# Performance work log

Measured on AMD Instinct MI355X. Metric: run time of the kernel, lower is better.

## Reference

```python
import jax, jax.numpy as jnp
import numpy as np

N, D, K = 32768, 256, 4096
COMMITMENT_COST = 0.25
EPS_NORM = 1e-12  # matches torch F.normalize eps


def _l2_normalize(x):
    n = jnp.linalg.norm(x, axis=1, keepdims=True)
    return x / jnp.maximum(n, EPS_NORM)


def setup_inputs() -> dict:
    key = jax.random.key(0)
    k1, k2 = jax.random.split(key)
    inputs = jax.random.normal(k1, (N, D), dtype=jnp.float32)
    # xavier_uniform-like scale for the codebook
    bound = float(np.sqrt(6.0 / (K + D)))
    embeddings = jax.random.uniform(k2, (K, D), dtype=jnp.float32, minval=-bound, maxval=bound)
    return {"inputs": inputs, "embeddings": embeddings}


def reference(inputs, embeddings):
    flat = inputs.reshape(-1, D)
    x = _l2_normalize(flat)              # [N, D]
    e = _l2_normalize(embeddings)        # [K, D]
    # squared euclidean distance on normalized vectors
    distances = (jnp.sum(x * x, axis=1, keepdims=True)
                 + jnp.sum(e * e, axis=1)
                 - 2.0 * jnp.matmul(x, e.T))          # [N, K]
    encoding_indices = jnp.argmin(distances, axis=1)  # [N]
    quantized = embeddings[encoding_indices]          # gather, [N, D]
    # commitment loss (EMA variant: only commitment term is trained)
    e_latent_loss = jnp.mean((jax.lax.stop_gradient(quantized) - flat) ** 2)
    loss = COMMITMENT_COST * e_latent_loss
    # straight-through estimator
    quantized_st = flat + jax.lax.stop_gradient(quantized - flat)
    quantized_st = quantized_st.reshape(inputs.shape)
    return quantized_st, loss, encoding_indices
```

## Files before the change

### kernel.cpp

```cpp
#include <hip/hip_runtime.h>
#include <math.h>
#include <stdint.h>
#include <limits.h>

#define NPTS 32768
#define DIM  256
#define KCB  4096
#define NQ   (NPTS*DIM)

#define EPSN    1e-12f
#define MARGIN1 6.0e-4f
#define F16MIN  6.103515625e-05f
#define CAPB    4096
#define KINIT   0x7F800000FFFFFFFFull

typedef __attribute__((ext_vector_type(8))) _Float16 f16x8;
typedef __attribute__((ext_vector_type(4))) _Float16 f16x4;
typedef __attribute__((ext_vector_type(4))) float    f32x4;

#define WS_EH0   0u
#define WS_TRI   2097152u
#define WS_SUME  4194304u
#define WS_EINV  4210688u
#define WS_XINV  4227072u
#define WS_IDX   4358144u
#define WS_RCB   4489216u
#define WS_RLB   4489232u
#define WS_BEST  4505616u
#define WS_LOSSP 4915232u

__device__ inline unsigned fbits(float f){ union{float f;unsigned u;}v; v.f=f; return v.u; }
__device__ inline float bitsf(unsigned u){ union{float f;unsigned u;}v; v.u=u; return v.f; }
__device__ inline uint64_t dbits(double d){ union{double d;uint64_t u;}v; v.d=d; return v.u; }
__device__ inline _Float16 g16(float v){
    return (fabsf(v) < F16MIN) ? (_Float16)0.0f : (_Float16)v;
}
__device__ inline void gload16(const void* src, void* lds){
    __builtin_amdgcn_global_load_lds((const __attribute__((address_space(1))) void*)src,
                                     (__attribute__((address_space(3))) void*)lds, 16, 0, 0);
}

__global__ __launch_bounds__(256) void k_norm(const float* __restrict__ x,
                                              const float* __restrict__ e,
                                              float* __restrict__ xinv,
                                              _Float16* __restrict__ eh0,
                                              float* __restrict__ sume,
                                              float* __restrict__ einv,
                                              int* __restrict__ rcb,
                                              uint64_t* __restrict__ bestu) {
    int w = threadIdx.x >> 6, l = threadIdx.x & 63;
    if (blockIdx.x < NPTS/4) {
        int row = blockIdx.x * 4 + w;
        float4 v = ((const float4*)x)[row * 64 + l];
        float s = v.x*v.x + v.y*v.y + v.z*v.z + v.w*v.w;
        #pragma unroll
        for (int o = 32; o; o >>= 1) s += __shfl_xor(s, o);
        if (l == 0) xinv[row] = 1.0f / fmaxf(sqrtf(s), EPSN);
    } else {
        int eb = blockIdx.x - NPTS/4;
        if (eb == 0 && threadIdx.x == 0) *rcb = 0;
        if (eb < 16) bestu[eb * 256 + threadIdx.x] = ~0ull;
        int row = eb * 4 + w;
        float4 v = ((const float4*)e)[row * 64 + l];
        float s = v.x*v.x + v.y*v.y + v.z*v.z + v.w*v.w;
        #pragma unroll
        for (int o = 32; o; o >>= 1) s += __shfl_xor(s, o);
        float inv = 1.0f / fmaxf(sqrtf(s), EPSN);
        float4 n = make_float4(v.x*inv, v.y*inv, v.z*inv, v.w*inv);
        f16x4 h0; h0[0]=g16(n.x); h0[1]=g16(n.y); h0[2]=g16(n.z); h0[3]=g16(n.w);
        ((f16x4*)eh0)[row * 64 + l] = h0;
        float s2 = n.x*n.x + n.y*n.y + n.z*n.z + n.w*n.w;
        #pragma unroll
        for (int o = 32; o; o >>= 1) s2 += __shfl_xor(s2, o);
        if (l == 0) { sume[row] = s2; einv[row] = inv; }
    }
}

__global__ __launch_bounds__(256,2) void k_phase1(
    const float* __restrict__ x, const float* __restrict__ xinv,
    const _Float16* __restrict__ eh0,
    ulonglong2* __restrict__ tri)
{
    __shared__ __align__(16) _Float16 Bs[2][32 * DIM];
    const int tid = threadIdx.x;
    const int w = tid >> 6, l = tid & 63;
    const int l15 = l & 15, lhi = l >> 4;
    const int rowbase = (blockIdx.x >> 2) * 256 + w * 64;
    const int kbase   = (blockIdx.x & 3) * 1024;
    char* BsC = (char*)&Bs[0][0];

    f16x8 a[4][8];
    #pragma unroll
    for (int g = 0; g < 4; g++) {
        int row = rowbase + g*16 + l15;
        float xv = xinv[row];
        const float4* xr = (const float4*)(x + row * DIM);
        #pragma unroll
        for (int dc = 0; dc < 8; dc++) {
            float4 f0 = xr[dc*8 + lhi*2];
            float4 f1 = xr[dc*8 + lhi*2 + 1];
            f16x8 av;
            av[0]=g16(f0.x*xv); av[1]=g16(f0.y*xv);
            av[2]=g16(f0.z*xv); av[3]=g16(f0.w*xv);
            av[4]=g16(f1.x*xv); av[5]=g16(f1.y*xv);
            av[6]=g16(f1.z*xv); av[7]=g16(f1.w*xv);
            a[g][dc] = av;
        }
    }

    uint64_t t0[4], t1[4];
    float d2[4];
    #pragma unroll
    for (int g = 0; g < 4; g++) { t0[g]=KINIT; t1[g]=KINIT; d2[g]=INFINITY; }

    const char* sbase = (const char*)eh0 + (size_t)kbase * 512
                      + (size_t)(l & 31) * 512 + w*32 + (l >> 5)*16;
    auto stage = [&](int kt, int bufbyte) {
        const char* s = sbase + kt * 16384;
        #pragma unroll
        for (int p = 0; p < 4; p++) {
            gload16(s + p*128, BsC + bufbyte + ((p*256 + w*64) << 4));
        }
    };

    const int rb = lhi*512 + l15*16;
    const f32x4 zc = (f32x4){0.f, 0.f, 0.f, 0.f};

    auto compute = [&](int kt, int bufbyte) {
        f32x4 acc[4][2];
        #pragma unroll
        for (int dc = 0; dc < 8; dc++) {
            #pragma unroll
            for (int ni = 0; ni < 2; ni++) {
                f16x8 b = *(const f16x8*)(BsC + bufbyte + dc*2048 + ni*256 + rb);
                if (dc == 0) {
                    acc[0][ni] = __builtin_amdgcn_mfma_f32_16x16x32_f16(b, a[0][0], zc, 0, 0, 0);
                    acc[1][ni] = __builtin_amdgcn_mfma_f32_16x16x32_f16(b, a[1][0], zc, 0, 0, 0);
                    acc[2][ni] = __builtin_amdgcn_mfma_f32_16x16x32_f16(b, a[2][0], zc, 0, 0, 0);
                    acc[3][ni] = __builtin_amdgcn_mfma_f32_16x16x32_f16(b, a[3][0], zc, 0, 0, 0);
                } else {
                    acc[0][ni] = __builtin_amdgcn_mfma_f32_16x16x32_f16(b, a[0][dc], acc[0][ni], 0, 0, 0);
                    acc[1][ni] = __builtin_amdgcn_mfma_f32_16x16x32_f16(b, a[1][dc], acc[1][ni], 0, 0, 0);
                    acc[2][ni] = __builtin_amdgcn_mfma_f32_16x16x32_f16(b, a[2][dc], acc[2][ni], 0, 0, 0);
                    acc[3][ni] = __builtin_amdgcn_mfma_f32_16x16x32_f16(b, a[3][dc], acc[3][ni], 0, 0, 0);
                }
            }
        }

        #pragma unroll
        for (int ni = 0; ni < 2; ni++) {
            #pragma unroll
            for (int g = 0; g < 4; g++) {
                f32x4 v = acc[g][ni];
                float mx = fmaxf(fmaxf(v[0], v[1]), fmaxf(v[2], v[3]));
                if (5.0f - 2.0f*mx < d2[g]) {
                    #pragma unroll
                    for (int r = 0; r < 4; r++) {
                        float db = 5.0f - 2.0f*v[r];
                        if (db < d2[g]) {
                            int code = kbase + kt*32 + ni*16 + lhi*4 + r;
                            uint64_t key = ((uint64_t)fbits(db) << 32) | (unsigned)code;
                            if (key < t1[g]) {
                                d2[g] = bitsf((unsigned)(t1[g] >> 32));
                                if (key < t0[g]) { t1[g] = t0[g]; t0[g] = key; }
                                else t1[g] = key;
                            } else {
                                d2[g] = db;
                            }
                        }
                    }
                }
            }
        }
    };

    stage(0, 0);
    for (int kt = 0; kt < 32; kt += 2) {
        __syncthreads();
        stage(kt + 1, 16384);
        compute(kt, 0);
        __syncthreads();
        if (kt + 2 < 32) stage(kt + 2, 0);
        compute(kt + 1, 16384);
    }

    #pragma unroll
    for (int g = 0; g < 4; g++) {
        uint64_t a0 = t0[g], a1 = t1[g];
        float a2 = d2[g];
        #pragma unroll
        for (int m = 16; m < 64; m <<= 1) {
            uint64_t b0 = __shfl_xor(a0, m), b1 = __shfl_xor(a1, m);
            float    b2 = __shfl_xor(a2, m);
            uint64_t lo  = a0 < b0 ? a0 : b0;
            uint64_t hi0 = a0 < b0 ? b0 : a0;
            uint64_t lo1 = a1 < b1 ? a1 : b1;
            uint64_t mid = hi0 > lo1 ? hi0 : lo1;
            a1 = hi0 < lo1 ? hi0 : lo1;
            a0 = lo;
            a2 = fminf(fminf(a2, b2), bitsf((unsigned)(mid >> 32)));
        }
        t0[g] = a0; t1[g] = a1; d2[g] = a2;
    }

    if (lhi == 0) {
        const int split = blockIdx.x & 3;
        #pragma unroll
        for (int g = 0; g < 4; g++) {
            int row = rowbase + g*16 + l15;
            float d0 = bitsf((unsigned)(t0[g] >> 32));
            uint64_t flag = (d2[g] - d0 < MARGIN1) ? (1ull << 12) : 0ull;
            ulonglong2 ent;
            ent.x = t0[g];
            ent.y = t1[g] | flag;
            tri[(row << 2) | split] = ent;
        }
    }
}

__global__ __launch_bounds__(256) void k_tailA(
    const ulonglong2* __restrict__ tri,
    const float* __restrict__ x, const float* __restrict__ emb,
    const float* __restrict__ xinv, const float* __restrict__ einv,
    const float* __restrict__ sume,
    int* __restrict__ idx,
    int* __restrict__ rcb, int* __restrict__ rlb)
{
    __shared__ int rowsA[256], ksA[256];
    __shared__ int cntA;
    const int tid = threadIdx.x;
    if (tid == 0) cntA = 0;
    __syncthreads();

    {
        int row = blockIdx.x * 256 + tid;
        ulonglong2 e0 = tri[row*4+0], e1 = tri[row*4+1],
                   e2 = tri[row*4+2], e3 = tri[row*4+3];
        uint64_t c0 = e0.x, c1 = e0.y & ~0x1000ull;
        float c2 = INFINITY;
        auto fold = [&](uint64_t b0, uint64_t b1) {
            b1 &= ~0x1000ull;
            uint64_t lo  = c0 < b0 ? c0 : b0;
            uint64_t hi0 = c0 < b0 ? b0 : c0;
            uint64_t lo1 = c1 < b1 ? c1 : b1;
            uint64_t mid = hi0 > lo1 ? hi0 : lo1;
            c1 = hi0 < lo1 ? hi0 : lo1;
            c0 = lo;
            c2 = fminf(c2, bitsf((unsigned)(mid >> 32)));
        };
        fold(e1.x, e1.y); fold(e2.x, e2.y); fold(e3.x, e3.y);
        int k0 = (int)((unsigned)c0 & 0xFFFu);
        idx[row] = k0;
        float d0 = bitsf((unsigned)(c0 >> 32));
        float d1 = bitsf((unsigned)(c1 >> 32));
        bool lA = (d1 - d0 < MARGIN1);
        bool lB = (c2 - d0 < MARGIN1);
        if ((e0.y >> 12) & 1) lB |= (bitsf((unsigned)(e0.x >> 32)) - d0 < MARGIN1);
        if ((e1.y >> 12) & 1) lB |= (bitsf((unsigned)(e1.x >> 32)) - d0 < MARGIN1);
        if ((e2.y >> 12) & 1) lB |= (bitsf((unsigned)(e2.x >> 32)) - d0 < MARGIN1);
        if ((e3.y >> 12) & 1) lB |= (bitsf((unsigned)(e3.x >> 32)) - d0 < MARGIN1);
        if (lA) {
            int k1 = (int)((unsigned)c1 & 0xFFFu);
            int p = atomicAdd(&cntA, 1);
            rowsA[p] = row; ksA[p] = k0 | (k1 << 12);
        }
        if (lB) {
            int q = atomicAdd(rcb, 1);
            if (q < CAPB) rlb[q] = row;
        }
    }
    __syncthreads();

    const int w = tid >> 6, l = tid & 63;
    const int nA = cntA;
    for (int i = w; i < nA; i += 4) {
        int row = rowsA[i];
        int k0 = ksA[i] & 0xFFF, k1 = (ksA[i] >> 12) & 0xFFF;
        float xv = xinv[row];
        float4 xf = ((const float4*)x)[row * 64 + l];
        double x0 = (double)xf.x * (double)xv, x1 = (double)xf.y * (double)xv;
        double x2 = (double)xf.z * (double)xv, x3 = (double)xf.w * (double)xv;
        int ks[2] = {k0, k1};
        double d[2];
        #pragma unroll
        for (int c = 0; c < 2; c++) {
            int k = ks[c];
            float ev = einv[k];
            float4 e4 = ((const float4*)emb)[k * 64 + l];
            d[c] = x0 * (double)(e4.x * ev) + x1 * (double)(e4.y * ev)
                 + x2 * (double)(e4.z * ev) + x3 * (double)(e4.w * ev);
        }
        #pragma unroll
        for (int o = 32; o; o >>= 1) {
            d[0] += __shfl_xor(d[0], o);
            d[1] += __shfl_xor(d[1], o);
        }
        if (l == 0) {
            double dist0 = 4.0 + (double)sume[k0] - 2.0 * d[0];
            double dist1 = 4.0 + (double)sume[k1] - 2.0 * d[1];
            uint64_t key0 = (dbits(dist0) & 0xFFFFFFFFFFFFF000ull) | (unsigned)k0;
            uint64_t key1 = (dbits(dist1) & 0xFFFFFFFFFFFFF000ull) | (unsigned)k1;
            idx[row] = (int)((key0 < key1 ? key0 : key1) & 0xFFFull);
        }
    }
}

__global__ __launch_bounds__(256) void k_full(
    const float* __restrict__ x, const float* __restrict__ emb,
    const float* __restrict__ xinv, const float* __restrict__ einv,
    const float* __restrict__ sume,
    const int* __restrict__ rcb, const int* __restrict__ rlb,
    uint64_t* __restrict__ bestu)
{
    __shared__ __align__(16) float xs[DIM];
    int cnt = *rcb; if (cnt > CAPB) cnt = CAPB; if (cnt <= 0) return;
    const int tid = threadIdx.x;
    const int grp = tid >> 3, sub = tid & 7;
    int items = cnt * 16;
    for (int item = blockIdx.x; item < items; item += gridDim.x) {
        int r = item >> 4, chunk = item & 15;
        int row = rlb[r];
        __syncthreads();
        xs[tid] = x[row * DIM + tid] * xinv[row];
        __syncthreads();
        const float4* xs4 = (const float4*)xs;
        uint64_t best = ~0ull;
        #pragma unroll
        for (int j = 0; j < 8; j++) {
            int k = chunk * 256 + grp * 8 + j;
            float ev = einv[k];
            const float4* e4 = (const float4*)(emb + (size_t)k * DIM);
            double dp0 = 0, dp1 = 0;
            #pragma unroll
            for (int i = 0; i < 8; i += 2) {
                float4 ef0 = e4[sub + i*8];
                float4 xf0 = xs4[sub + i*8];
                float4 ef1 = e4[sub + (i+1)*8];
                float4 xf1 = xs4[sub + (i+1)*8];
                dp0 += (double)xf0.x * (double)(ef0.x * ev)
                     + (double)xf0.y * (double)(ef0.y * ev)
                     + (double)xf0.z * (double)(ef0.z * ev)
                     + (double)xf0.w * (double)(ef0.w * ev);
                dp1 += (double)xf1.x * (double)(ef1.x * ev)
                     + (double)xf1.y * (double)(ef1.y * ev)
                     + (double)xf1.z * (double)(ef1.z * ev)
                     + (double)xf1.w * (double)(ef1.w * ev);
            }
            double dp = dp0 + dp1;
            #pragma unroll
            for (int o = 4; o; o >>= 1) dp += __shfl_xor(dp, o);
            if (sub == 0) {
                double dist = 4.0 + (double)sume[k] - 2.0 * dp;
                uint64_t key = (dbits(dist) & 0xFFFFFFFFFFFFF000ull) | (unsigned)k;
                best = key < best ? key : best;
            }
        }
        if (sub == 0)
            atomicMin((unsigned long long*)&bestu[r], (unsigned long long)best);
    }
}

__global__ __launch_bounds__(256) void k_ffin(const int* __restrict__ rcb,
                                              const int* __restrict__ rlb,
                                              const uint64_t* __restrict__ bestu,
                                              int* __restrict__ idx) {
    int cnt = *rcb; if (cnt > CAPB) cnt = CAPB;
    int i = blockIdx.x * 256 + threadIdx.x;
    if (i < cnt) idx[rlb[i]] = (int)(bestu[i] & 0xFFFull);
}

__global__ __launch_bounds__(256) void k_gather(const float* __restrict__ x,
                                                const float* __restrict__ emb,
                                                const int* __restrict__ idx,
                                                float* __restrict__ out,
                                                float* __restrict__ lossp) {
    int t = blockIdx.x * 256 + threadIdx.x;
    float ls = 0.f;
    #pragma unroll
    for (int s = 0; s < 4; ++s) {
        int i4 = t + s * 524288;
        int n = i4 >> 6, c4 = i4 & 63;
        int id = idx[n];
        float4 f = ((const float4*)x)[i4];
        float4 q = ((const float4*)emb)[id * 64 + c4];
        float dx = q.x - f.x, dy = q.y - f.y, dz = q.z - f.z, dw = q.w - f.w;
        float4 o = make_float4(f.x + dx, f.y + dy, f.z + dz, f.w + dw);
        ((float4*)out)[i4] = o;
        ls += dx*dx + dy*dy + dz*dz + dw*dw;
        if (c4 == 0) out[NQ + 1 + n] = (float)id;
    }
    #pragma unroll
    for (int o = 32; o; o >>= 1) ls += __shfl_xor(ls, o);
    __shared__ float wsum[4];
    int wid = threadIdx.x >> 6, lane = threadIdx.x & 63;
    if (lane == 0) wsum[wid] = ls;
    __syncthreads();
    if (threadIdx.x == 0) lossp[blockIdx.x] = wsum[0] + wsum[1] + wsum[2] + wsum[3];
}

__global__ __launch_bounds__(256) void k_finalize(const float* __restrict__ lossp,
                                                  float* __restrict__ out) {
    double s = 0;
    for (int i = threadIdx.x; i < 2048; i += 256) s += (double)lossp[i];
    #pragma unroll
    for (int o = 32; o; o >>= 1) s += __shfl_xor(s, o);
    __shared__ double wd[4];
    int wid = threadIdx.x >> 6, lane = threadIdx.x & 63;
    if (lane == 0) wd[wid] = s;
    __syncthreads();
    if (threadIdx.x == 0)
        out[NQ] = (float)(0.25 * ((wd[0] + wd[1] + wd[2] + wd[3]) / (double)NQ));
}

extern "C" void kernel_launch(void* const* d_in, const int* in_sizes, int n_in,
                              void* d_out, int out_size, void* d_ws, size_t ws_size,
                              hipStream_t stream) {
    const float* x   = (const float*)d_in[0];
    const float* emb = (const float*)d_in[1];
    char* ws = (char*)d_ws;
    _Float16* eh0 = (_Float16*)(ws + WS_EH0);
    ulonglong2* tri = (ulonglong2*)(ws + WS_TRI);
    float* sume  = (float*)(ws + WS_SUME);
    float* einv  = (float*)(ws + WS_EINV);
    float* xinv  = (float*)(ws + WS_XINV);
    int*   idx   = (int*)  (ws + WS_IDX);
    int*   rcb   = (int*)  (ws + WS_RCB);
    int*   rlb   = (int*)  (ws + WS_RLB);
    uint64_t* bestu = (uint64_t*)(ws + WS_BEST);
    float* lossp = (float*)(ws + WS_LOSSP);
    float* out = (float*)d_out;

    hipLaunchKernelGGL(k_norm,     dim3(NPTS/4 + KCB/4), dim3(256), 0, stream,
                       x, emb, xinv, eh0, sume, einv, rcb, bestu);
    hipLaunchKernelGGL(k_phase1,   dim3(NPTS/256*4),     dim3(256), 0, stream,
                       x, xinv, eh0, tri);
    hipLaunchKernelGGL(k_tailA,    dim3(NPTS/256),       dim3(256), 0, stream,
                       tri, x, emb, xinv, einv, sume, idx, rcb, rlb);
    hipLaunchKernelGGL(k_full,     dim3(2048),           dim3(256), 0, stream,
                       x, emb, xinv, einv, sume, rcb, rlb, bestu);
    hipLaunchKernelGGL(k_ffin,     dim3(16),             dim3(256), 0, stream, rcb, rlb, bestu, idx);
    hipLaunchKernelGGL(k_gather,   dim3(2048),           dim3(256), 0, stream,
                       x, emb, idx, out, lossp);
    hipLaunchKernelGGL(k_finalize, dim3(1),              dim3(256), 0, stream, lossp, out);
}
```

Baseline: 171.5 us.

## Precompute fp16 normalized inputs and split codebook search eight ways

Adds an fp16 copy of the normalized input rows, written by the norm kernel into the output buffer as scratch, so phase1 loads fp16 fragments directly instead of reloading fp32 and converting. Phase1 now splits the codebook into eight 512-code slices instead of four, doubling the block count to improve occupancy and load balance. The per-row partial results also move into the output buffer and are merged over eight entries in tailA. This trades extra scratch traffic and a longer merge for more parallelism, and relies on the output buffer being overwritten later by k_gather.

```diff
diff --git a/kernel.cpp b/kernel.cpp
--- a/kernel.cpp
+++ b/kernel.cpp
@@ -13,13 +13,13 @@
 #define F16MIN  6.103515625e-05f
 #define CAPB    4096
 #define KINIT   0x7F800000FFFFFFFFull
+#define NSPLIT  8
 
 typedef __attribute__((ext_vector_type(8))) _Float16 f16x8;
 typedef __attribute__((ext_vector_type(4))) _Float16 f16x4;
 typedef __attribute__((ext_vector_type(4))) float    f32x4;
 
 #define WS_EH0   0u
-#define WS_TRI   2097152u
 #define WS_SUME  4194304u
 #define WS_EINV  4210688u
 #define WS_XINV  4227072u
@@ -28,6 +28,7 @@
 #define WS_RLB   4489232u
 #define WS_BEST  4505616u
 #define WS_LOSSP 4915232u
+#define DOUT_TRI 16777216u
 
 __device__ inline unsigned fbits(float f){ union{float f;unsigned u;}v; v.f=f; return v.u; }
 __device__ inline float bitsf(unsigned u){ union{float f;unsigned u;}v; v.u=u; return v.f; }
@@ -43,6 +44,7 @@
 __global__ __launch_bounds__(256) void k_norm(const float* __restrict__ x,
                                               const float* __restrict__ e,
                                               float* __restrict__ xinv,
+                                              _Float16* __restrict__ xh,
                                               _Float16* __restrict__ eh0,
                                               float* __restrict__ sume,
                                               float* __restrict__ einv,
@@ -55,7 +57,11 @@
         float s = v.x*v.x + v.y*v.y + v.z*v.z + v.w*v.w;
         #pragma unroll
         for (int o = 32; o; o >>= 1) s += __shfl_xor(s, o);
-        if (l == 0) xinv[row] = 1.0f / fmaxf(sqrtf(s), EPSN);
+        float inv = 1.0f / fmaxf(sqrtf(s), EPSN);
+        if (l == 0) xinv[row] = inv;
+        f16x4 h;
+        h[0]=g16(v.x*inv); h[1]=g16(v.y*inv); h[2]=g16(v.z*inv); h[3]=g16(v.w*inv);
+        ((f16x4*)xh)[row * 64 + l] = h;
     } else {
         int eb = blockIdx.x - NPTS/4;
         if (eb == 0 && threadIdx.x == 0) *rcb = 0;
@@ -77,7 +83,7 @@
 }
 
 __global__ __launch_bounds__(256,2) void k_phase1(
-    const float* __restrict__ x, const float* __restrict__ xinv,
+    const _Float16* __restrict__ xh,
     const _Float16* __restrict__ eh0,
     ulonglong2* __restrict__ tri)
 {
@@ -85,27 +91,17 @@
     const int tid = threadIdx.x;
     const int w = tid >> 6, l = tid & 63;
     const int l15 = l & 15, lhi = l >> 4;
-    const int rowbase = (blockIdx.x >> 2) * 256 + w * 64;
-    const int kbase   = (blockIdx.x & 3) * 1024;
+    const int rowbase = (blockIdx.x >> 3) * 256 + w * 64;
+    const int kbase   = (blockIdx.x & 7) * 512;
     char* BsC = (char*)&Bs[0][0];
 
     f16x8 a[4][8];
     #pragma unroll
     for (int g = 0; g < 4; g++) {
-        int row = rowbase + g*16 + l15;
-        float xv = xinv[row];
-        const float4* xr = (const float4*)(x + row * DIM);
-        #pragma unroll
-        for (int dc = 0; dc < 8; dc++) {
-            float4 f0 = xr[dc*8 + lhi*2];
-            float4 f1 = xr[dc*8 + lhi*2 + 1];
-            f16x8 av;
-            av[0]=g16(f0.x*xv); av[1]=g16(f0.y*xv);
-            av[2]=g16(f0.z*xv); av[3]=g16(f0.w*xv);
-            av[4]=g16(f1.x*xv); av[5]=g16(f1.y*xv);
-            av[6]=g16(f1.z*xv); av[7]=g16(f1.w*xv);
-            a[g][dc] = av;
-        }
+        const _Float16* xr = xh + (size_t)(rowbase + g*16 + l15) * DIM;
+        #pragma unroll
+        for (int dc = 0; dc < 8; dc++)
+            a[g][dc] = *(const f16x8*)(xr + dc*32 + lhi*8);
     }
 
     uint64_t t0[4], t1[4];
@@ -175,12 +171,12 @@
     };
 
     stage(0, 0);
-    for (int kt = 0; kt < 32; kt += 2) {
+    for (int kt = 0; kt < 16; kt += 2) {
         __syncthreads();
         stage(kt + 1, 16384);
         compute(kt, 0);
         __syncthreads();
-        if (kt + 2 < 32) stage(kt + 2, 0);
+        if (kt + 2 < 16) stage(kt + 2, 0);
         compute(kt + 1, 16384);
     }
 
@@ -204,7 +200,7 @@
     }
 
     if (lhi == 0) {
-        const int split = blockIdx.x & 3;
+        const int split = blockIdx.x & 7;
         #pragma unroll
         for (int g = 0; g < 4; g++) {
             int row = rowbase + g*16 + l15;
@@ -213,7 +209,7 @@
             ulonglong2 ent;
             ent.x = t0[g];
             ent.y = t1[g] | flag;
-            tri[(row << 2) | split] = ent;
+            tri[(row << 3) | split] = ent;
         }
     }
 }
@@ -234,12 +230,15 @@
 
     {
         int row = blockIdx.x * 256 + tid;
-        ulonglong2 e0 = tri[row*4+0], e1 = tri[row*4+1],
-                   e2 = tri[row*4+2], e3 = tri[row*4+3];
-        uint64_t c0 = e0.x, c1 = e0.y & ~0x1000ull;
+        ulonglong2 e[NSPLIT];
+        #pragma unroll
+        for (int s = 0; s < NSPLIT; s++) e[s] = tri[row*NSPLIT + s];
+        uint64_t c0 = e[0].x, c1 = e[0].y & ~0x1000ull;
         float c2 = INFINITY;
-        auto fold = [&](uint64_t b0, uint64_t b1) {
-            b1 &= ~0x1000ull;
+        #pragma unroll
+        for (int s = 1; s < NSPLIT; s++) {
+            uint64_t b0 = e[s].x;
+            uint64_t b1 = e[s].y & ~0x1000ull;
             uint64_t lo  = c0 < b0 ? c0 : b0;
             uint64_t hi0 = c0 < b0 ? b0 : c0;
             uint64_t lo1 = c1 < b1 ? c1 : b1;
@@ -247,18 +246,18 @@
             c1 = hi0 < lo1 ? hi0 : lo1;
             c0 = lo;
             c2 = fminf(c2, bitsf((unsigned)(mid >> 32)));
-        };
-        fold(e1.x, e1.y); fold(e2.x, e2.y); fold(e3.x, e3.y);
+        }
         int k0 = (int)((unsigned)c0 & 0xFFFu);
         idx[row] = k0;
         float d0 = bitsf((unsigned)(c0 >> 32));
         float d1 = bitsf((unsigned)(c1 >> 32));
         bool lA = (d1 - d0 < MARGIN1);
         bool lB = (c2 - d0 < MARGIN1);
-        if ((e0.y >> 12) & 1) lB |= (bitsf((unsigned)(e0.x >> 32)) - d0 < MARGIN1);
-        if ((e1.y >> 12) & 1) lB |= (bitsf((unsigned)(e1.x >> 32)) - d0 < MARGIN1);
-        if ((e2.y >> 12) & 1) lB |= (bitsf((unsigned)(e2.x >> 32)) - d0 < MARGIN1);
-        if ((e3.y >> 12) & 1) lB |= (bitsf((unsigned)(e3.x >> 32)) - d0 < MARGIN1);
+        #pragma unroll
+        for (int s = 0; s < NSPLIT; s++) {
+            if ((e[s].y >> 12) & 1)
+                lB |= (bitsf((unsigned)(e[s].x >> 32)) - d0 < MARGIN1);
+        }
         if (lA) {
             int k1 = (int)((unsigned)c1 & 0xFFFu);
             int p = atomicAdd(&cntA, 1);
@@ -419,7 +418,8 @@
     const float* emb = (const float*)d_in[1];
     char* ws = (char*)d_ws;
     _Float16* eh0 = (_Float16*)(ws + WS_EH0);
-    ulonglong2* tri = (ulonglong2*)(ws + WS_TRI);
+    _Float16* xh  = (_Float16*)d_out;
+    ulonglong2* tri = (ulonglong2*)((char*)d_out + DOUT_TRI);
     float* sume  = (float*)(ws + WS_SUME);
     float* einv  = (float*)(ws + WS_EINV);
     float* xinv  = (float*)(ws + WS_XINV);
@@ -430,16 +430,16 @@
     float* lossp = (float*)(ws + WS_LOSSP);
     float* out = (float*)d_out;
 
-    hipLaunchKernelGGL(k_norm,     dim3(NPTS/4 + KCB/4), dim3(256), 0, stream,
-                       x, emb, xinv, eh0, sume, einv, rcb, bestu);
-    hipLaunchKernelGGL(k_phase1,   dim3(NPTS/256*4),     dim3(256), 0, stream,
-                       x, xinv, eh0, tri);
-    hipLaunchKernelGGL(k_tailA,    dim3(NPTS/256),       dim3(256), 0, stream,
+    hipLaunchKernelGGL(k_norm,     dim3(NPTS/4 + KCB/4),     dim3(256), 0, stream,
+                       x, emb, xinv, xh, eh0, sume, einv, rcb, bestu);
+    hipLaunchKernelGGL(k_phase1,   dim3(NPTS/256*NSPLIT),    dim3(256), 0, stream,
+                       xh, eh0, tri);
+    hipLaunchKernelGGL(k_tailA,    dim3(NPTS/256),           dim3(256), 0, stream,
                        tri, x, emb, xinv, einv, sume, idx, rcb, rlb);
-    hipLaunchKernelGGL(k_full,     dim3(2048),           dim3(256), 0, stream,
+    hipLaunchKernelGGL(k_full,     dim3(2048),               dim3(256), 0, stream,
                        x, emb, xinv, einv, sume, rcb, rlb, bestu);
-    hipLaunchKernelGGL(k_ffin,     dim3(16),             dim3(256), 0, stream, rcb, rlb, bestu, idx);
-    hipLaunchKernelGGL(k_gather,   dim3(2048),           dim3(256), 0, stream,
+    hipLaunchKernelGGL(k_ffin,     dim3(16),                 dim3(256), 0, stream, rcb, rlb, bestu, idx);
+    hipLaunchKernelGGL(k_gather,   dim3(2048),               dim3(256), 0, stream,
                        x, emb, idx, out, lossp);
-    hipLaunchKernelGGL(k_finalize, dim3(1),              dim3(256), 0, stream, lossp, out);
-}
+    hipLaunchKernelGGL(k_finalize, dim3(1),                  dim3(256), 0, stream, lossp, out);
+}
```

New measurement: 174.3 us. About the same (+1.7%).
